# Kernel optimization log

Hardware: AMD Instinct MI355X
Metric: run time of the kernel (lower is better)

Reference implementation:

```python
import jax, jax.numpy as jnp
import numpy as np

N_NODES = 50000
N_EDGES = 800000
FT = 128
HID = 128
N_EXTRA_LAYERS = 2  # num_layers - 1


def _gin_conv(x, src, dst, W1, b1, W2, b2):
    # GINConv with eps=0: mlp(x + sum_{j->i} x_j)
    agg = jax.ops.segment_sum(x[src], dst, num_segments=N_NODES)
    h = x + agg
    h = jax.nn.relu(h @ W1 + b1)
    return h @ W2 + b2


def setup_inputs() -> dict:
    key = jax.random.key(0)
    ks = jax.random.split(key, 12)
    feat = jax.random.normal(ks[0], (N_NODES, FT), dtype=jnp.float32)
    edge_index = jax.random.randint(ks[1], (2, N_EDGES), 0, N_NODES, dtype=jnp.int32)
    s = 0.02
    # layer 0: ft -> hid
    W1a = jax.random.normal(ks[2], (FT, HID), dtype=jnp.float32) * s
    b1a = jnp.zeros((HID,), dtype=jnp.float32)
    W2a = jax.random.normal(ks[3], (HID, HID), dtype=jnp.float32) * s
    b2a = jnp.zeros((HID,), dtype=jnp.float32)
    # remaining layers stacked: [L, hid, hid]
    Ws1 = jax.random.normal(ks[4], (N_EXTRA_LAYERS, HID, HID), dtype=jnp.float32) * s
    bs1 = jnp.zeros((N_EXTRA_LAYERS, HID), dtype=jnp.float32)
    Ws2 = jax.random.normal(ks[5], (N_EXTRA_LAYERS, HID, HID), dtype=jnp.float32) * s
    bs2 = jnp.zeros((N_EXTRA_LAYERS, HID), dtype=jnp.float32)
    return {"feat": feat, "edge_index": edge_index,
            "W1a": W1a, "b1a": b1a, "W2a": W2a, "b2a": b2a,
            "Ws1": Ws1, "bs1": bs1, "Ws2": Ws2, "bs2": bs2}


def reference(feat, edge_index, W1a, b1a, W2a, b2a, Ws1, bs1, Ws2, bs2):
    src = edge_index[0]
    dst = edge_index[1]
    x = jax.nn.relu(_gin_conv(feat, src, dst, W1a, b1a, W2a, b2a))
    for i in range(N_EXTRA_LAYERS):
        x = jax.nn.relu(_gin_conv(x, src, dst, Ws1[i], bs1[i], Ws2[i], bs2[i]))
    return x[None]  # [1, N, hid]
```

## Files before the change

### kernel.cpp

```cpp
#include <hip/hip_runtime.h>
#include <hip/hip_bf16.h>

#define N_NODES 50000
#define N_EDGES 800000
#define HID 128

typedef __attribute__((ext_vector_type(8))) short bf16x8;
typedef __attribute__((ext_vector_type(4))) float f32x4;

__device__ inline ushort f32_to_bf16_bits(float v) {
    union { float f; unsigned u; } a; a.f = v;
    unsigned r = a.u + 0x7fff + ((a.u >> 16) & 1);
    return (ushort)(r >> 16);
}
__device__ inline float bf16bits_to_f32(ushort b) {
    union { float f; unsigned u; } a; a.u = ((unsigned)b) << 16;
    return a.f;
}


__global__ __launch_bounds__(256) void hist_kernel(const int* __restrict__ dst,
                                                   int* __restrict__ cnt) {
    int e = blockIdx.x * 256 + threadIdx.x;
    if (e < N_EDGES) atomicAdd(&cnt[dst[e]], 1);
}

__global__ __launch_bounds__(256) void alloc_offsets_kernel(const int* __restrict__ cnt,
                                                            int* __restrict__ offs,
                                                            int* __restrict__ cursor,
                                                            int* __restrict__ gcur) {
    int i = blockIdx.x * 256 + threadIdx.x;
    int lane = threadIdx.x & 63;
    int c = (i < N_NODES) ? cnt[i] : 0;
    int pre = c;
    #pragma unroll
    for (int d = 1; d < 64; d <<= 1) {
        int t = __shfl_up(pre, d);
        if (lane >= d) pre += t;
    }
    int base = 0;
    if (lane == 63) base = atomicAdd(gcur, pre);
    base = __shfl(base, 63);
    int o = base + pre - c;
    if (i < N_NODES) { offs[i] = o; cursor[i] = o; }
}

__global__ __launch_bounds__(256) void scatter_kernel(const int* __restrict__ src,
                                                      const int* __restrict__ dst,
                                                      int* __restrict__ cursor,
                                                      int* __restrict__ csr) {
    int e = blockIdx.x * 256 + threadIdx.x;
    if (e < N_EDGES) {
        int d = dst[e];
        int pos = atomicAdd(&cursor[d], 1);
        csr[pos] = src[e];
    }
}


__global__ __launch_bounds__(256) void prep_kernel(const float* __restrict__ W1a,
                                                   const float* __restrict__ W2a,
                                                   const float* __restrict__ Ws1,
                                                   const float* __restrict__ Ws2,
                                                   short* __restrict__ whi,
                                                   short* __restrict__ wlo) {
    int mat = blockIdx.y;
    const float* W;
    switch (mat) {
        case 0: W = W1a; break;
        case 1: W = W2a; break;
        case 2: W = Ws1; break;
        case 3: W = Ws2; break;
        case 4: W = Ws1 + HID * HID; break;
        default: W = Ws2 + HID * HID; break;
    }
    int tid2 = blockIdx.x * 256 + threadIdx.x;
    int l = tid2 & 63;
    int ft = tid2 >> 6;
    int t = ft & 3, f = ft >> 2;
    int g = l >> 4, lm = l & 15;
    bf16x8 hv, lv;
    #pragma unroll
    for (int i = 0; i < 8; ++i) {
        int k = t * 32 + g * 8 + i;
        int n = f * 16 + lm;
        float v = W[k * HID + n];
        ushort hb = f32_to_bf16_bits(v);
        ushort lb = f32_to_bf16_bits(v - bf16bits_to_f32(hb));
        hv[i] = (short)hb;
        lv[i] = (short)lb;
    }
    size_t base = ((size_t)mat * 2048 + tid2) * 8;
    *(bf16x8*)&whi[base] = hv;
    *(bf16x8*)&wlo[base] = lv;
}


__global__ __launch_bounds__(64) void fused_gin_kernel(const float* __restrict__ x,
                                                       const int* __restrict__ csr,
                                                       const int* __restrict__ offs,
                                                       const int* __restrict__ cnt,
                                                       const short* __restrict__ w1hi,
                                                       const short* __restrict__ w1lo,
                                                       const short* __restrict__ w2hi,
                                                       const short* __restrict__ w2lo,
                                                       const float* __restrict__ b1,
                                                       const float* __restrict__ b2,
                                                       float* __restrict__ xout) {
    __shared__ short sHi[16][136];
    __shared__ short sLo[16][136];

    const int lane = threadIdx.x;
    const int nbase = blockIdx.x * 16;
    const int g = lane >> 4, lm = lane & 15;
    const float2* x2 = (const float2*)x;

    for (int n = 0; n < 16; ++n) {
        int node = nbase + n;
        int off = offs[node];
        int c = cnt[node];
        float2 acc = x2[(size_t)node * 64 + lane];
        int e = 0;
        for (; e + 8 <= c; e += 8) {
            int s[8];
            #pragma unroll
            for (int q = 0; q < 8; ++q) s[q] = csr[off + e + q];
            float2 v[8];
            #pragma unroll
            for (int q = 0; q < 8; ++q) v[q] = x2[(size_t)s[q] * 64 + lane];
            acc.x += ((v[0].x + v[1].x) + (v[2].x + v[3].x)) +
                     ((v[4].x + v[5].x) + (v[6].x + v[7].x));
            acc.y += ((v[0].y + v[1].y) + (v[2].y + v[3].y)) +
                     ((v[4].y + v[5].y) + (v[6].y + v[7].y));
        }
        for (; e + 4 <= c; e += 4) {
            int s0 = csr[off + e], s1 = csr[off + e + 1];
            int s2 = csr[off + e + 2], s3 = csr[off + e + 3];
            float2 v0 = x2[(size_t)s0 * 64 + lane];
            float2 v1 = x2[(size_t)s1 * 64 + lane];
            float2 v2 = x2[(size_t)s2 * 64 + lane];
            float2 v3 = x2[(size_t)s3 * 64 + lane];
            acc.x += (v0.x + v1.x) + (v2.x + v3.x);
            acc.y += (v0.y + v1.y) + (v2.y + v3.y);
        }
        for (; e < c; ++e) {
            int s = csr[off + e];
            float2 v = x2[(size_t)s * 64 + lane];
            acc.x += v.x;
            acc.y += v.y;
        }
        ushort hx = f32_to_bf16_bits(acc.x);
        ushort lx = f32_to_bf16_bits(acc.x - bf16bits_to_f32(hx));
        ushort hy = f32_to_bf16_bits(acc.y);
        ushort ly = f32_to_bf16_bits(acc.y - bf16bits_to_f32(hy));
        *(unsigned*)&sHi[n][2 * lane] = (unsigned)hx | ((unsigned)hy << 16);
        *(unsigned*)&sLo[n][2 * lane] = (unsigned)lx | ((unsigned)ly << 16);
    }

    f32x4 accT[8];

    {
        bf16x8 ahi[4], alo[4];
        #pragma unroll
        for (int t = 0; t < 4; ++t) {
            ahi[t] = *(bf16x8*)&sHi[lm][t * 32 + g * 8];
            alo[t] = *(bf16x8*)&sLo[lm][t * 32 + g * 8];
        }
        #pragma unroll
        for (int f = 0; f < 8; ++f) {
            const bf16x8* bh = (const bf16x8*)&w1hi[((size_t)(f * 4) * 64 + lane) * 8];
            const bf16x8* bl = (const bf16x8*)&w1lo[((size_t)(f * 4) * 64 + lane) * 8];
            f32x4 acc = {0.f, 0.f, 0.f, 0.f};
            #pragma unroll
            for (int t = 0; t < 4; ++t) {
                bf16x8 bhv = bh[t * 64];
                bf16x8 blv = bl[t * 64];
                acc = __builtin_amdgcn_mfma_f32_16x16x32_bf16(ahi[t], bhv, acc, 0, 0, 0);
                acc = __builtin_amdgcn_mfma_f32_16x16x32_bf16(alo[t], bhv, acc, 0, 0, 0);
                acc = __builtin_amdgcn_mfma_f32_16x16x32_bf16(ahi[t], blv, acc, 0, 0, 0);
            }
            accT[f] = acc;
        }
    }
    #pragma unroll
    for (int f = 0; f < 8; ++f) {
        float bv = b1[f * 16 + lm];
        #pragma unroll
        for (int r = 0; r < 4; ++r) {
            float v = accT[f][r] + bv;
            v = v > 0.f ? v : 0.f;
            ushort hb = f32_to_bf16_bits(v);
            ushort lb = f32_to_bf16_bits(v - bf16bits_to_f32(hb));
            int m = g * 4 + r;
            sHi[m][f * 16 + lm] = (short)hb;
            sLo[m][f * 16 + lm] = (short)lb;
        }
    }

    {
        bf16x8 ahi[4], alo[4];
        #pragma unroll
        for (int t = 0; t < 4; ++t) {
            ahi[t] = *(bf16x8*)&sHi[lm][t * 32 + g * 8];
            alo[t] = *(bf16x8*)&sLo[lm][t * 32 + g * 8];
        }
        #pragma unroll
        for (int f = 0; f < 8; ++f) {
            const bf16x8* bh = (const bf16x8*)&w2hi[((size_t)(f * 4) * 64 + lane) * 8];
            const bf16x8* bl = (const bf16x8*)&w2lo[((size_t)(f * 4) * 64 + lane) * 8];
            f32x4 acc = {0.f, 0.f, 0.f, 0.f};
            #pragma unroll
            for (int t = 0; t < 4; ++t) {
                bf16x8 bhv = bh[t * 64];
                bf16x8 blv = bl[t * 64];
                acc = __builtin_amdgcn_mfma_f32_16x16x32_bf16(ahi[t], bhv, acc, 0, 0, 0);
                acc = __builtin_amdgcn_mfma_f32_16x16x32_bf16(alo[t], bhv, acc, 0, 0, 0);
                acc = __builtin_amdgcn_mfma_f32_16x16x32_bf16(ahi[t], blv, acc, 0, 0, 0);
            }
            accT[f] = acc;
        }
    }
    #pragma unroll
    for (int f = 0; f < 8; ++f) {
        float bv = b2[f * 16 + lm];
        #pragma unroll
        for (int r = 0; r < 4; ++r) {
            float v = accT[f][r] + bv;
            v = v > 0.f ? v : 0.f;
            int gn = nbase + g * 4 + r;
            xout[(size_t)gn * HID + f * 16 + lm] = v;
        }
    }
}


extern "C" void kernel_launch(void* const* d_in, const int* in_sizes, int n_in,
                              void* d_out, int out_size, void* d_ws, size_t ws_size,
                              hipStream_t stream) {
    const float* feat = (const float*)d_in[0];
    const int* edge = (const int*)d_in[1];
    const int* src = edge;
    const int* dst = edge + N_EDGES;
    const float* W1a = (const float*)d_in[2];
    const float* b1a = (const float*)d_in[3];
    const float* W2a = (const float*)d_in[4];
    const float* b2a = (const float*)d_in[5];
    const float* Ws1 = (const float*)d_in[6];
    const float* bs1 = (const float*)d_in[7];
    const float* Ws2 = (const float*)d_in[8];
    const float* bs2 = (const float*)d_in[9];
    float* out = (float*)d_out;

    int* cnt = (int*)d_ws;
    int* offs = cnt + 50176;
    int* cursor = offs + 50176;
    int* gcur = cursor + 50176;
    int* csr = gcur + 64;
    float* xb0 = (float*)(csr + N_EDGES);
    float* xb1 = xb0 + (size_t)N_NODES * HID;
    short* whi = (short*)(xb1 + (size_t)N_NODES * HID);
    short* wlo = whi + 6 * 2048 * 8;

    hipMemsetAsync(cnt, 0, N_NODES * sizeof(int), stream);
    hipMemsetAsync(gcur, 0, sizeof(int), stream);

    const int EB = (N_EDGES + 255) / 256;
    const int NB = (N_NODES + 255) / 256;
    prep_kernel<<<dim3(8, 6), 256, 0, stream>>>(W1a, W2a, Ws1, Ws2, whi, wlo);
    hist_kernel<<<EB, 256, 0, stream>>>(dst, cnt);
    alloc_offsets_kernel<<<NB, 256, 0, stream>>>(cnt, offs, cursor, gcur);
    scatter_kernel<<<EB, 256, 0, stream>>>(src, dst, cursor, csr);

    const int FB = N_NODES / 16;
    const int MS = 16384;

    fused_gin_kernel<<<FB, 64, 0, stream>>>(feat, csr, offs, cnt,
                                            whi + 0 * MS, wlo + 0 * MS,
                                            whi + 1 * MS, wlo + 1 * MS, b1a, b2a, xb0);
    fused_gin_kernel<<<FB, 64, 0, stream>>>(xb0, csr, offs, cnt,
                                            whi + 2 * MS, wlo + 2 * MS,
                                            whi + 3 * MS, wlo + 3 * MS, bs1, bs2, xb1);
    fused_gin_kernel<<<FB, 64, 0, stream>>>(xb1, csr, offs, cnt,
                                            whi + 4 * MS, wlo + 4 * MS,
                                            whi + 5 * MS, wlo + 5 * MS,
                                            bs1 + HID, bs2 + HID, out);
}
```

Measured before the change: 385.4 us.

## Store node features as bf16 and split each GIN block across four waves

```diff
diff --git a/kernel.cpp b/kernel.cpp
--- a/kernel.cpp
+++ b/kernel.cpp
@@ -55,6 +55,22 @@
         int pos = atomicAdd(&cursor[d], 1);
         csr[pos] = src[e];
     }
+}
+
+
+__global__ __launch_bounds__(256) void conv_kernel(const float* __restrict__ in,
+                                                   ushort* __restrict__ out) {
+    int t = blockIdx.x * 256 + threadIdx.x;
+    if (t >= (N_NODES * HID) / 8) return;
+    const float4* in4 = (const float4*)in;
+    float4 a = in4[2 * t], b = in4[2 * t + 1];
+    float v[8] = {a.x, a.y, a.z, a.w, b.x, b.y, b.z, b.w};
+    uint4 o;
+    o.x = (unsigned)f32_to_bf16_bits(v[0]) | ((unsigned)f32_to_bf16_bits(v[1]) << 16);
+    o.y = (unsigned)f32_to_bf16_bits(v[2]) | ((unsigned)f32_to_bf16_bits(v[3]) << 16);
+    o.z = (unsigned)f32_to_bf16_bits(v[4]) | ((unsigned)f32_to_bf16_bits(v[5]) << 16);
+    o.w = (unsigned)f32_to_bf16_bits(v[6]) | ((unsigned)f32_to_bf16_bits(v[7]) << 16);
+    ((uint4*)out)[t] = o;
 }
 
 
@@ -96,68 +112,77 @@
 }
 
 
-__global__ __launch_bounds__(64) void fused_gin_kernel(const float* __restrict__ x,
-                                                       const int* __restrict__ csr,
-                                                       const int* __restrict__ offs,
-                                                       const int* __restrict__ cnt,
-                                                       const short* __restrict__ w1hi,
-                                                       const short* __restrict__ w1lo,
-                                                       const short* __restrict__ w2hi,
-                                                       const short* __restrict__ w2lo,
-                                                       const float* __restrict__ b1,
-                                                       const float* __restrict__ b2,
-                                                       float* __restrict__ xout) {
+__global__ __launch_bounds__(256) void fused_gin_kernel(const unsigned* __restrict__ xbf,
+                                                        const int* __restrict__ csr,
+                                                        const int* __restrict__ offs,
+                                                        const int* __restrict__ cnt,
+                                                        const short* __restrict__ w1hi,
+                                                        const short* __restrict__ w1lo,
+                                                        const short* __restrict__ w2hi,
+                                                        const short* __restrict__ w2lo,
+                                                        const float* __restrict__ b1,
+                                                        const float* __restrict__ b2,
+                                                        ushort* __restrict__ xoutb,
+                                                        float* __restrict__ xoutf) {
     __shared__ short sHi[16][136];
     __shared__ short sLo[16][136];
 
-    const int lane = threadIdx.x;
+    const int tid = threadIdx.x;
+    const int lane = tid & 63;
+    const int wid = tid >> 6;
     const int nbase = blockIdx.x * 16;
     const int g = lane >> 4, lm = lane & 15;
-    const float2* x2 = (const float2*)x;
-
-    for (int n = 0; n < 16; ++n) {
-        int node = nbase + n;
+
+    for (int n = 0; n < 4; ++n) {
+        int node = nbase + wid * 4 + n;
         int off = offs[node];
         int c = cnt[node];
-        float2 acc = x2[(size_t)node * 64 + lane];
+        unsigned su = xbf[(size_t)node * 64 + lane];
+        float ax = __uint_as_float(su << 16);
+        float ay = __uint_as_float(su & 0xffff0000u);
         int e = 0;
         for (; e + 8 <= c; e += 8) {
             int s[8];
             #pragma unroll
             for (int q = 0; q < 8; ++q) s[q] = csr[off + e + q];
-            float2 v[8];
-            #pragma unroll
-            for (int q = 0; q < 8; ++q) v[q] = x2[(size_t)s[q] * 64 + lane];
-            acc.x += ((v[0].x + v[1].x) + (v[2].x + v[3].x)) +
-                     ((v[4].x + v[5].x) + (v[6].x + v[7].x));
-            acc.y += ((v[0].y + v[1].y) + (v[2].y + v[3].y)) +
-                     ((v[4].y + v[5].y) + (v[6].y + v[7].y));
+            unsigned u[8];
+            #pragma unroll
+            for (int q = 0; q < 8; ++q) u[q] = xbf[(size_t)s[q] * 64 + lane];
+            #pragma unroll
+            for (int q = 0; q < 8; ++q) {
+                ax += __uint_as_float(u[q] << 16);
+                ay += __uint_as_float(u[q] & 0xffff0000u);
+            }
         }
         for (; e + 4 <= c; e += 4) {
             int s0 = csr[off + e], s1 = csr[off + e + 1];
             int s2 = csr[off + e + 2], s3 = csr[off + e + 3];
-            float2 v0 = x2[(size_t)s0 * 64 + lane];
-            float2 v1 = x2[(size_t)s1 * 64 + lane];
-            float2 v2 = x2[(size_t)s2 * 64 + lane];
-            float2 v3 = x2[(size_t)s3 * 64 + lane];
-            acc.x += (v0.x + v1.x) + (v2.x + v3.x);
-            acc.y += (v0.y + v1.y) + (v2.y + v3.y);
+            unsigned u0 = xbf[(size_t)s0 * 64 + lane];
+            unsigned u1 = xbf[(size_t)s1 * 64 + lane];
+            unsigned u2 = xbf[(size_t)s2 * 64 + lane];
+            unsigned u3 = xbf[(size_t)s3 * 64 + lane];
+            ax += (__uint_as_float(u0 << 16) + __uint_as_float(u1 << 16)) +
+                  (__uint_as_float(u2 << 16) + __uint_as_float(u3 << 16));
+            ay += (__uint_as_float(u0 & 0xffff0000u) + __uint_as_float(u1 & 0xffff0000u)) +
+                  (__uint_as_float(u2 & 0xffff0000u) + __uint_as_float(u3 & 0xffff0000u));
         }
         for (; e < c; ++e) {
             int s = csr[off + e];
-            float2 v = x2[(size_t)s * 64 + lane];
-            acc.x += v.x;
-            acc.y += v.y;
-        }
-        ushort hx = f32_to_bf16_bits(acc.x);
-        ushort lx = f32_to_bf16_bits(acc.x - bf16bits_to_f32(hx));
-        ushort hy = f32_to_bf16_bits(acc.y);
-        ushort ly = f32_to_bf16_bits(acc.y - bf16bits_to_f32(hy));
-        *(unsigned*)&sHi[n][2 * lane] = (unsigned)hx | ((unsigned)hy << 16);
-        *(unsigned*)&sLo[n][2 * lane] = (unsigned)lx | ((unsigned)ly << 16);
-    }
-
-    f32x4 accT[8];
+            unsigned u = xbf[(size_t)s * 64 + lane];
+            ax += __uint_as_float(u << 16);
+            ay += __uint_as_float(u & 0xffff0000u);
+        }
+        ushort hx = f32_to_bf16_bits(ax);
+        ushort lx = f32_to_bf16_bits(ax - bf16bits_to_f32(hx));
+        ushort hy = f32_to_bf16_bits(ay);
+        ushort ly = f32_to_bf16_bits(ay - bf16bits_to_f32(hy));
+        int row = wid * 4 + n;
+        *(unsigned*)&sHi[row][2 * lane] = (unsigned)hx | ((unsigned)hy << 16);
+        *(unsigned*)&sLo[row][2 * lane] = (unsigned)lx | ((unsigned)ly << 16);
+    }
+    __syncthreads();
+
+    f32x4 accT[2];
 
     {
         bf16x8 ahi[4], alo[4];
@@ -166,8 +191,10 @@
             ahi[t] = *(bf16x8*)&sHi[lm][t * 32 + g * 8];
             alo[t] = *(bf16x8*)&sLo[lm][t * 32 + g * 8];
         }
-        #pragma unroll
-        for (int f = 0; f < 8; ++f) {
+        __syncthreads();
+        #pragma unroll
+        for (int ff = 0; ff < 2; ++ff) {
+            int f = wid * 2 + ff;
             const bf16x8* bh = (const bf16x8*)&w1hi[((size_t)(f * 4) * 64 + lane) * 8];
             const bf16x8* bl = (const bf16x8*)&w1lo[((size_t)(f * 4) * 64 + lane) * 8];
             f32x4 acc = {0.f, 0.f, 0.f, 0.f};
@@ -179,15 +206,16 @@
                 acc = __builtin_amdgcn_mfma_f32_16x16x32_bf16(alo[t], bhv, acc, 0, 0, 0);
                 acc = __builtin_amdgcn_mfma_f32_16x16x32_bf16(ahi[t], blv, acc, 0, 0, 0);
             }
-            accT[f] = acc;
+            accT[ff] = acc;
         }
     }
     #pragma unroll
-    for (int f = 0; f < 8; ++f) {
+    for (int ff = 0; ff < 2; ++ff) {
+        int f = wid * 2 + ff;
         float bv = b1[f * 16 + lm];
         #pragma unroll
         for (int r = 0; r < 4; ++r) {
-            float v = accT[f][r] + bv;
+            float v = accT[ff][r] + bv;
             v = v > 0.f ? v : 0.f;
             ushort hb = f32_to_bf16_bits(v);
             ushort lb = f32_to_bf16_bits(v - bf16bits_to_f32(hb));
@@ -196,6 +224,7 @@
             sLo[m][f * 16 + lm] = (short)lb;
         }
     }
+    __syncthreads();
 
     {
         bf16x8 ahi[4], alo[4];
@@ -205,7 +234,8 @@
             alo[t] = *(bf16x8*)&sLo[lm][t * 32 + g * 8];
         }
         #pragma unroll
-        for (int f = 0; f < 8; ++f) {
+        for (int ff = 0; ff < 2; ++ff) {
+            int f = wid * 2 + ff;
             const bf16x8* bh = (const bf16x8*)&w2hi[((size_t)(f * 4) * 64 + lane) * 8];
             const bf16x8* bl = (const bf16x8*)&w2lo[((size_t)(f * 4) * 64 + lane) * 8];
             f32x4 acc = {0.f, 0.f, 0.f, 0.f};
@@ -217,18 +247,21 @@
                 acc = __builtin_amdgcn_mfma_f32_16x16x32_bf16(alo[t], bhv, acc, 0, 0, 0);
                 acc = __builtin_amdgcn_mfma_f32_16x16x32_bf16(ahi[t], blv, acc, 0, 0, 0);
             }
-            accT[f] = acc;
+            accT[ff] = acc;
         }
     }
     #pragma unroll
-    for (int f = 0; f < 8; ++f) {
+    for (int ff = 0; ff < 2; ++ff) {
+        int f = wid * 2 + ff;
         float bv = b2[f * 16 + lm];
         #pragma unroll
         for (int r = 0; r < 4; ++r) {
-            float v = accT[f][r] + bv;
+            float v = accT[ff][r] + bv;
             v = v > 0.f ? v : 0.f;
             int gn = nbase + g * 4 + r;
-            xout[(size_t)gn * HID + f * 16 + lm] = v;
+            size_t gi = (size_t)gn * HID + f * 16 + lm;
+            if (xoutb) xoutb[gi] = f32_to_bf16_bits(v);
+            if (xoutf) xoutf[gi] = v;
         }
     }
 }
@@ -256,9 +289,9 @@
     int* cursor = offs + 50176;
     int* gcur = cursor + 50176;
     int* csr = gcur + 64;
-    float* xb0 = (float*)(csr + N_EDGES);
-    float* xb1 = xb0 + (size_t)N_NODES * HID;
-    short* whi = (short*)(xb1 + (size_t)N_NODES * HID);
+    ushort* xbA = (ushort*)(csr + N_EDGES);
+    ushort* xbB = xbA + (size_t)N_NODES * HID;
+    short* whi = (short*)(xbB + (size_t)N_NODES * HID);
     short* wlo = whi + 6 * 2048 * 8;
 
     hipMemsetAsync(cnt, 0, N_NODES * sizeof(int), stream);
@@ -266,6 +299,7 @@
 
     const int EB = (N_EDGES + 255) / 256;
     const int NB = (N_NODES + 255) / 256;
+    conv_kernel<<<3125, 256, 0, stream>>>(feat, xbA);
     prep_kernel<<<dim3(8, 6), 256, 0, stream>>>(W1a, W2a, Ws1, Ws2, whi, wlo);
     hist_kernel<<<EB, 256, 0, stream>>>(dst, cnt);
     alloc_offsets_kernel<<<NB, 256, 0, stream>>>(cnt, offs, cursor, gcur);
@@ -274,14 +308,17 @@
     const int FB = N_NODES / 16;
     const int MS = 16384;
 
-    fused_gin_kernel<<<FB, 64, 0, stream>>>(feat, csr, offs, cnt,
-                                            whi + 0 * MS, wlo + 0 * MS,
-                                            whi + 1 * MS, wlo + 1 * MS, b1a, b2a, xb0);
-    fused_gin_kernel<<<FB, 64, 0, stream>>>(xb0, csr, offs, cnt,
-                                            whi + 2 * MS, wlo + 2 * MS,
-                                            whi + 3 * MS, wlo + 3 * MS, bs1, bs2, xb1);
-    fused_gin_kernel<<<FB, 64, 0, stream>>>(xb1, csr, offs, cnt,
-                                            whi + 4 * MS, wlo + 4 * MS,
-                                            whi + 5 * MS, wlo + 5 * MS,
-                                            bs1 + HID, bs2 + HID, out);
-}
+    fused_gin_kernel<<<FB, 256, 0, stream>>>((const unsigned*)xbA, csr, offs, cnt,
+                                             whi + 0 * MS, wlo + 0 * MS,
+                                             whi + 1 * MS, wlo + 1 * MS, b1a, b2a,
+                                             xbB, nullptr);
+    fused_gin_kernel<<<FB, 256, 0, stream>>>((const unsigned*)xbB, csr, offs, cnt,
+                                             whi + 2 * MS, wlo + 2 * MS,
+                                             whi + 3 * MS, wlo + 3 * MS, bs1, bs2,
+                                             xbA, nullptr);
+    fused_gin_kernel<<<FB, 256, 0, stream>>>((const unsigned*)xbA, csr, offs, cnt,
+                                             whi + 4 * MS, wlo + 4 * MS,
+                                             whi + 5 * MS, wlo + 5 * MS,
+                                             bs1 + HID, bs2 + HID,
+                                             nullptr, out);
+}
```

Result: faster. 331.9 us (-13.9%).
